# Optimization experiments

Hardware: AMD Instinct MI355X
Metric: run time of the kernel (lower is better)

## Reference

```python
import jax, jax.numpy as jnp
import numpy as np

CLIP_VAL = 32

def setup_inputs() -> dict:
    key = jax.random.key(0)
    ks = jax.random.split(key, 8)
    B, T, D_MODEL, H, DK = 4, 1024, 1024, 16, 64
    s = 0.02  # small init scale, glorot-like magnitude
    return {
        "query": jax.random.normal(ks[0], (B, T, D_MODEL), jnp.float32),
        "value": jax.random.normal(ks[1], (B, T, D_MODEL), jnp.float32),
        "W_Q": jax.random.normal(ks[2], (H, D_MODEL, DK), jnp.float32) * s,
        "W_K": jax.random.normal(ks[3], (H, D_MODEL, DK), jnp.float32) * s,
        "W_V": jax.random.normal(ks[4], (H, D_MODEL, DK), jnp.float32) * s,
        "W_O": jax.random.normal(ks[5], (H, DK, D_MODEL), jnp.float32) * s,
        "emb_Q": jax.random.normal(ks[6], (2 * CLIP_VAL + 1, DK), jnp.float32) * s,
        "emb_S": jax.random.normal(ks[7], (2 * CLIP_VAL + 1, DK), jnp.float32) * s,
    }

def reference(query, value, W_Q, W_K, W_V, W_O, emb_Q, emb_S):
    # query/value: (B, T, D_Model); per-head weights: (H, D_Model, Dk)
    T = query.shape[1]
    Dk = W_Q.shape[-1]
    sqrt_D = jnp.sqrt(jnp.asarray(Dk, query.dtype))

    # relative position index matrix: (T, T) ints in [0, 2*clip]
    tau = jnp.arange(T)
    rel = (jnp.clip(tau[None, :] - tau[:, None], -CLIP_VAL, CLIP_VAL) + CLIP_VAL)
    eQ = emb_Q[rel]  # (T, T, Dk) relative key embedding
    eS = emb_S[rel]  # (T, T, Dv) relative value embedding

    qW = jnp.einsum('btm,hmd->bhtd', query, W_Q)  # (B,H,T,Dk)
    kW = jnp.einsum('btm,hmd->bhtd', value, W_K)
    vW = jnp.einsum('btm,hmd->bhtd', value, W_V)

    # content scores + relative-query bias, both scaled by 1/sqrt(Dk)
    scores = (jnp.einsum('bhtd,bhsd->bhts', qW, kW)
              + jnp.einsum('bhtd,tsd->bhts', qW, eQ)) / sqrt_D
    p = jax.nn.softmax(scores, axis=-1)  # (B,H,T,T)

    # value combination + relative-value term
    heads = (jnp.einsum('bhts,bhsd->bhtd', p, vW)
             + jnp.einsum('bhts,tsd->bhtd', p, eS))

    # per-head output projection then sum over heads
    out = jnp.einsum('bhtd,hdm->btm', heads, W_O)  # (B,T,D_Model)
    return out
```

## Files before the change

### kernel.cpp

```cpp
#include <hip/hip_runtime.h>
#include <math.h>


typedef _Float16 f16;
typedef f16 half8 __attribute__((ext_vector_type(8)));
typedef f16 half4v __attribute__((ext_vector_type(4)));
typedef float f32x4 __attribute__((ext_vector_type(4)));
typedef float f32x16 __attribute__((ext_vector_type(16)));

__global__ __launch_bounds__(256) void prep(
    const float* __restrict__ q, const float* __restrict__ v,
    const float* __restrict__ W0, const float* __restrict__ W1,
    const float* __restrict__ W2, const float* __restrict__ WO,
    f16* __restrict__ q16, f16* __restrict__ Wt16, f16* __restrict__ WOt16) {
    __shared__ float tile[64][65];
    const int bx = blockIdx.x;
    const int t = threadIdx.x;
    if (bx < 8192) {
        int i = (bx * 256 + t) * 4;
        const float* s = (i < 4194304) ? (q + i) : (v + (i - 4194304));
        float4 x = *(const float4*)s;
        half4v h = {(f16)x.x, (f16)x.y, (f16)x.z, (f16)x.w};
        *(half4v*)&q16[i] = h;
        return;
    }
    const int c = t & 63, r4 = t >> 6;
    const int n = t >> 2, kc = (t & 3) * 16;
    if (bx < 8960) {
        const int idx = bx - 8192;
        const int z = idx >> 4, k0 = (idx & 15) * 64;
        const float* src = ((z < 16) ? W0 : (z < 32) ? W1 : W2) + (size_t)(z & 15) * 65536;
        f16* out = Wt16 + (size_t)z * 65536;
#pragma unroll
        for (int p = 0; p < 16; ++p)
            tile[r4 + p * 4][c] = src[(size_t)(k0 + r4 + p * 4) * 64 + c];
        __syncthreads();
        f16 buf[16];
#pragma unroll
        for (int i = 0; i < 16; ++i) buf[i] = (f16)tile[kc + i][n];
        *(half8*)&out[(size_t)n * 1024 + k0 + kc] = *(half8*)&buf[0];
        *(half8*)&out[(size_t)n * 1024 + k0 + kc + 8] = *(half8*)&buf[8];
        return;
    }
    {
        const int idx = bx - 8960;
        const int k0 = (idx & 15) * 64, n0 = (idx >> 4) * 64;
#pragma unroll
        for (int p = 0; p < 16; ++p)
            tile[r4 + p * 4][c] = WO[(size_t)(k0 + r4 + p * 4) * 1024 + n0 + c];
        __syncthreads();
        f16 buf[16];
#pragma unroll
        for (int i = 0; i < 16; ++i) buf[i] = (f16)tile[kc + i][n];
        *(half8*)&WOt16[(size_t)(n0 + n) * 1024 + k0 + kc] = *(half8*)&buf[0];
        *(half8*)&WOt16[(size_t)(n0 + n) * 1024 + k0 + kc + 8] = *(half8*)&buf[8];
    }
}

template <int MODE, int NT, bool DBUF>
__global__ __launch_bounds__(256) void mfma_gemm(
    const f16* __restrict__ Aq, const f16* __restrict__ Av,
    const f16* __restrict__ Bt, float* __restrict__ C,
    f16* __restrict__ oQ, f16* __restrict__ oK, f16* __restrict__ oVt) {
    constexpr int K = 1024;
    constexpr int NI = NT / 32;
    constexpr int LDSZ = (128 + NT) * 64;
    const int n0 = blockIdx.x * NT;
    const int m0 = blockIdx.y * 128;
    const f16* Abase = (MODE == 0) ? ((n0 < 1024) ? Aq : Av) : Aq;

    __shared__ f16 lds[LDSZ * (DBUF ? 2 : 1)];

    const int tid = threadIdx.x;
    const int l = tid & 63, wv = tid >> 6;
    const int rseg = l >> 3;
    const int g = (l & 7) ^ rseg;
    const bool isA = (wv < 2);
    const int rowBase = isA ? (wv & 1) * 64 : (wv & 1) * (NT / 2);
    const int nLoads = isA ? 8 : (NT / 16);
    const f16* gSrc = isA ? (Abase + (size_t)m0 * K) : (Bt + (size_t)n0 * K);
    const f16* gLane = gSrc + (size_t)(rowBase + rseg) * K + g * 8;
    const int ldsRow0 = (isA ? 0 : 128) + rowBase;

    const int fr = l & 15, fq = l >> 4, sw = fr & 7;
    const int mi2 = wv & 1, ni2 = wv >> 1;
    int aOff[NI], bOff[4];
#pragma unroll
    for (int i = 0; i < 4; ++i) bOff[i] = (mi2 * 64 + i * 16 + fr) * 128;
#pragma unroll
    for (int i = 0; i < NI; ++i)
        aOff[i] = (128 + ni2 * (NT / 2) + i * 16 + fr) * 128;

    f32x4 acc[4][NI];
#pragma unroll
    for (int i = 0; i < 4; ++i)
#pragma unroll
        for (int j = 0; j < NI; ++j) acc[i][j] = {0.f, 0.f, 0.f, 0.f};

    auto issue = [&](int k0, int buf) {
        f16* dst = lds + (buf ? LDSZ : 0);
#pragma unroll 8
        for (int i = 0; i < nLoads; ++i) {
            const f16* src = gLane + (size_t)i * 8 * K + k0;
            __builtin_amdgcn_global_load_lds(
                (const __attribute__((address_space(1))) unsigned int*)src,
                (__attribute__((address_space(3))) unsigned int*)
                    &dst[(ldsRow0 + i * 8) * 64], 16, 0, 0);
        }
    };

    if (DBUF) issue(0, 0);
    int it = 0;
    for (int k0 = 0; k0 < K; k0 += 64, ++it) {
        if (!DBUF) issue(k0, 0);
        __syncthreads();
        if (DBUF && k0 + 64 < K) issue(k0 + 64, (it + 1) & 1);
        const char* lp = (const char*)lds + (DBUF ? (it & 1) * (LDSZ * 2) : 0);
#pragma unroll
        for (int kk = 0; kk < 2; ++kk) {
            const int glq = kk * 4 + fq;
            const int sgl = (glq ^ sw) * 16;
            half8 aF[NI], bF[4];
#pragma unroll
            for (int i = 0; i < NI; ++i)
                aF[i] = *(const half8*)(lp + aOff[i] + sgl);
#pragma unroll
            for (int i = 0; i < 4; ++i)
                bF[i] = *(const half8*)(lp + bOff[i] + sgl);
#pragma unroll
            for (int mi = 0; mi < 4; ++mi)
#pragma unroll
                for (int ni = 0; ni < NI; ++ni)
                    acc[mi][ni] = __builtin_amdgcn_mfma_f32_16x16x32_f16(
                        aF[ni], bF[mi], acc[mi][ni], 0, 0, 0);
        }
        if (!DBUF) __syncthreads();
    }
#pragma unroll
    for (int mi = 0; mi < 4; ++mi) {
        const int m = m0 + mi2 * 64 + mi * 16 + fr;
#pragma unroll
        for (int ni = 0; ni < NI; ++ni) {
            const int n = n0 + ni2 * (NT / 2) + ni * 16 + 4 * fq;
            if (MODE == 1) {
                *(f32x4*)(C + (size_t)m * 1024 + n) = acc[mi][ni];
            } else {
                const int w = n >> 10, h = (n >> 6) & 15, d = n & 63;
                const int b = m >> 10, t = m & 1023;
                const size_t bh = (size_t)(b * 16 + h);
                f32x4 a = acc[mi][ni];
                if (w == 0) {
                    half4v hv = {(f16)(a[0] * 0.125f), (f16)(a[1] * 0.125f),
                                 (f16)(a[2] * 0.125f), (f16)(a[3] * 0.125f)};
                    *(half4v*)&oQ[bh * 65536 + (size_t)t * 64 + d] = hv;
                } else if (w == 1) {
                    half4v hv = {(f16)a[0], (f16)a[1], (f16)a[2], (f16)a[3]};
                    *(half4v*)&oK[bh * 65536 + (size_t)t * 64 + d] = hv;
                } else {
#pragma unroll
                    for (int r = 0; r < 4; ++r)
                        oVt[bh * 65536 + (size_t)(d + r) * 1024 + t] = (f16)a[r];
                }
            }
        }
    }
}

__global__ __launch_bounds__(256, 2) void attn_kernel(
    const f16* __restrict__ q16a, const f16* __restrict__ k16,
    const f16* __restrict__ vt16, const float* __restrict__ embQ,
    const float* __restrict__ embS, f16* __restrict__ heads16) {
    const int bh = blockIdx.x;
    const int t0 = blockIdx.y * 128;
    const f16* qg = q16a + (size_t)bh * 65536;
    const f16* kg = k16 + (size_t)bh * 65536;
    const f16* vg = vt16 + (size_t)bh * 65536;

    __shared__ f16 Kt[2][4096];
    __shared__ f16 Vt[2][4096];
    __shared__ f16 qEl[66 * 136];
    __shared__ f16 band[128 * 72];
    __shared__ float e64s[64];

    const int tid = threadIdx.x;
    const int wv = tid >> 6, lane = tid & 63;
    const int tl32 = lane & 31, h = lane >> 5;
    const int tl = wv * 32 + tl32;
    const int tg = t0 + tl;

    auto stageKV = [&](int j0, int buf) {
#pragma unroll
        for (int i = 0; i < 2; ++i) {
            const int rt = wv * 16 + i * 8 + (lane >> 3);
            const int g = (lane & 7) ^ (rt & 7);
            __builtin_amdgcn_global_load_lds(
                (const __attribute__((address_space(1))) unsigned int*)
                    (kg + (size_t)(j0 + rt) * 64 + g * 8),
                (__attribute__((address_space(3))) unsigned int*)
                    &Kt[buf][(wv * 16 + i * 8) * 64], 16, 0, 0);
            __builtin_amdgcn_global_load_lds(
                (const __attribute__((address_space(1))) unsigned int*)
                    (vg + (size_t)rt * 1024 + j0 + g * 8),
                (__attribute__((address_space(3))) unsigned int*)
                    &Vt[buf][(wv * 16 + i * 8) * 64], 16, 0, 0);
        }
    };

    half8 qf[4];
#pragma unroll
    for (int ks = 0; ks < 4; ++ks)
        qf[ks] = *(const half8*)&qg[(size_t)tg * 64 + (2 * ks + h) * 8];
    stageKV(0, 0);

    f16* embQs = band;
    for (int idx = tid; idx < 768; idx += 256) {
        const int row = idx >> 3, p = idx & 7, g = p ^ (row & 7);
        half8 hv;
        if (row < 65) {
            const float* s = embQ + row * 64 + g * 8;
#pragma unroll
            for (int j = 0; j < 8; ++j) hv[j] = (f16)s[j];
        } else {
#pragma unroll
            for (int j = 0; j < 8; ++j) hv[j] = (f16)0.f;
        }
        *(half8*)&embQs[row * 64 + p * 8] = hv;
    }
    __syncthreads();
    {
        f32x16 qacc[3];
#pragma unroll
        for (int mt = 0; mt < 3; ++mt)
#pragma unroll
            for (int r = 0; r < 16; ++r) qacc[mt][r] = 0.f;
#pragma unroll
        for (int ks = 0; ks < 4; ++ks)
#pragma unroll
            for (int mt = 0; mt < 3; ++mt) {
                const int row = tl32 + 32 * mt;
                const int p = (2 * ks + h) ^ (row & 7);
                half8 ef = *(const half8*)&embQs[row * 64 + p * 8];
                qacc[mt] = __builtin_amdgcn_mfma_f32_32x32x16_f16(
                    ef, qf[ks], qacc[mt], 0, 0, 0);
            }
        __syncthreads();
#pragma unroll
        for (int mt = 0; mt < 3; ++mt)
#pragma unroll
            for (int r = 0; r < 16; ++r) {
                const int rr = (r & 3) + 8 * (r >> 2) + 4 * h + 32 * mt;
                if (rr < 65) qEl[rr * 136 + tl] = (f16)qacc[mt][r];
            }
    }
    for (int idx = tid; idx < 1152; idx += 256) {
        half8 hv;
#pragma unroll
        for (int j = 0; j < 8; ++j) hv[j] = (f16)(-1.0e4f);
        *(half8*)&band[idx * 8] = hv;
    }
    if (tid < 64) e64s[tid] = embS[64 * 64 + tid];
    __syncthreads();
    const float qE0 = (float)qEl[tl];
    const float qE64 = (float)qEl[64 * 136 + tl];

    float rs = 0.f, rsL = 0.f;
    f32x16 oacc[2];
#pragma unroll
    for (int dt = 0; dt < 2; ++dt)
#pragma unroll
        for (int r = 0; r < 16; ++r) oacc[dt][r] = 0.f;

    for (int jt = 0; jt < 16; ++jt) {
        const int j0 = jt * 64;
        __syncthreads();
        if (jt < 15) stageKV(j0 + 64, (jt + 1) & 1);
        const f16* Ktc = Kt[jt & 1];
        const f16* Vtc = Vt[jt & 1];
        f32x16 sacc[2];
#pragma unroll
        for (int mt = 0; mt < 2; ++mt)
#pragma unroll
            for (int r = 0; r < 16; ++r) sacc[mt][r] = 0.f;
#pragma unroll
        for (int ks = 0; ks < 4; ++ks)
#pragma unroll
            for (int mt = 0; mt < 2; ++mt) {
                const int row = tl32 + 32 * mt;
                const int p = (2 * ks + h) ^ (row & 7);
                half8 kf = *(const half8*)&Ktc[row * 64 + p * 8];
                sacc[mt] = __builtin_amdgcn_mfma_f32_32x32x16_f16(
                    kf, qf[ks], sacc[mt], 0, 0, 0);
            }
        const int dj = j0 - t0;
        if (dj <= -128 || dj >= 192) {
            const float bias = (dj < 0) ? qE0 : qE64;
            float ts = 0.f;
#pragma unroll
            for (int mt = 0; mt < 2; ++mt)
#pragma unroll
                for (int r = 0; r < 16; ++r) {
                    float pe = __expf(sacc[mt][r] + bias);
                    sacc[mt][r] = pe; ts += pe;
                }
            rs += ts;
            if (dj < 0) rsL += ts;
        } else {
#pragma unroll
            for (int mt = 0; mt < 2; ++mt)
#pragma unroll
                for (int r = 0; r < 16; ++r) {
                    const int sg = j0 + 32 * mt + (r & 3) + 8 * (r >> 2) + 4 * h;
                    const int ds = sg - tg;
                    const int dc = ds < -32 ? -32 : (ds > 32 ? 32 : ds);
                    float v = sacc[mt][r] + (float)qEl[(dc + 32) * 136 + tl];
                    if (ds >= -31 && ds <= 31) band[tl * 72 + ds + 31] = (f16)v;
                    float pe = __expf(v);
                    sacc[mt][r] = pe; rs += pe;
                    if (ds <= -32) rsL += pe;
                }
        }
#pragma unroll
        for (int ks = 0; ks < 4; ++ks) {
            const int mtile = ks >> 1, rb = (ks & 1) * 8;
            float ex[4];
#pragma unroll
            for (int c = 0; c < 4; ++c) {
                float send = (h == 0) ? sacc[mtile][rb + 4 + c]
                                      : sacc[mtile][rb + c];
                ex[c] = __shfl_xor(send, 32);
            }
            half8 pf;
#pragma unroll
            for (int j = 0; j < 4; ++j)
                pf[j] = (f16)((h == 0) ? sacc[mtile][rb + j] : ex[j]);
#pragma unroll
            for (int j = 0; j < 4; ++j)
                pf[4 + j] = (f16)((h == 0) ? ex[j] : sacc[mtile][rb + 4 + j]);
#pragma unroll
            for (int dt = 0; dt < 2; ++dt) {
                const int row = tl32 + 32 * dt;
                const int p = (2 * ks + h) ^ (row & 7);
                half8 vf = *(const half8*)&Vtc[row * 64 + p * 8];
                oacc[dt] = __builtin_amdgcn_mfma_f32_32x32x16_f16(
                    vf, pf, oacc[dt], 0, 0, 0);
            }
        }
    }
    rs += __shfl_xor(rs, 32);
    rsL += __shfl_xor(rsL, 32);
    float sumBand = 0.f;
#pragma unroll
    for (int c = 0; c < 4; ++c) {
        const int kb = 32 * h + 8 * c;
        half8 bv = *(const half8*)&band[tl * 72 + kb];
        half8 ev;
#pragma unroll
        for (int j = 0; j < 8; ++j) {
            const int k = kb + j;
            float v;
            if (k == 63) v = rsL;
            else { v = __expf((float)bv[j]); sumBand += v; }
            ev[j] = (f16)v;
        }
        *(half8*)&band[tl * 72 + kb] = ev;
    }
    sumBand += __shfl_xor(sumBand, 32);
    const float sumR = rs - rsL - sumBand;
    for (int idx = tid; idx < 512; idx += 256) {
        const int d = idx >> 3, p = idx & 7, g = p ^ (d & 7);
        half8 hv;
#pragma unroll
        for (int j = 0; j < 8; ++j) {
            const int k = g * 8 + j;
            hv[j] = (f16)embS[((k == 63) ? 0 : (k + 1)) * 64 + d];
        }
        *(half8*)&Kt[0][d * 64 + p * 8] = hv;
    }
    __syncthreads();
#pragma unroll
    for (int ks = 0; ks < 4; ++ks) {
        half8 pf = *(const half8*)&band[tl * 72 + 16 * ks + 8 * h];
#pragma unroll
        for (int dt = 0; dt < 2; ++dt) {
            const int row = tl32 + 32 * dt;
            const int p = (2 * ks + h) ^ (row & 7);
            half8 ef = *(const half8*)&Kt[0][row * 64 + p * 8];
            oacc[dt] = __builtin_amdgcn_mfma_f32_32x32x16_f16(
                ef, pf, oacc[dt], 0, 0, 0);
        }
    }
    __syncthreads();
    const float inv = 1.0f / rs;
#pragma unroll
    for (int dt = 0; dt < 2; ++dt)
#pragma unroll
        for (int r = 0; r < 16; ++r) {
            const int d = (r & 3) + 8 * (r >> 2) + 4 * h + 32 * dt;
            band[tl * 72 + d] = (f16)((oacc[dt][r] + sumR * e64s[d]) * inv);
        }
    __syncthreads();
    const int b = bh >> 4, hh = bh & 15;
    const int row = tid >> 1, cb = (tid & 1) * 32;
    f16* dst = heads16 + ((size_t)(b * 1024 + t0 + row) * 1024) + hh * 64 + cb;
#pragma unroll
    for (int c = 0; c < 4; ++c)
        *(half8*)&dst[c * 8] = *(const half8*)&band[row * 72 + cb + c * 8];
}

extern "C" void kernel_launch(void* const* d_in, const int* in_sizes, int n_in,
                              void* d_out, int out_size, void* d_ws, size_t ws_size,
                              hipStream_t stream) {
    const float* query = (const float*)d_in[0];
    const float* value = (const float*)d_in[1];
    const float* WQ   = (const float*)d_in[2];
    const float* WK   = (const float*)d_in[3];
    const float* WV   = (const float*)d_in[4];
    const float* WO   = (const float*)d_in[5];
    const float* embQ = (const float*)d_in[6];
    const float* embS = (const float*)d_in[7];
    float* out = (float*)d_out;

    f16* w0    = (f16*)d_ws;
    f16* q16   = w0;
    f16* v16   = w0 + 4194304;
    f16* Wt16  = w0 + 8388608;
    f16* WOt16 = w0 + 11534336;
    f16* q16a  = w0 + 12582912;
    f16* k16   = w0 + 16777216;
    f16* vt16  = w0 + 20971520;
    f16* h16   = w0 + 25165824;

    prep<<<9216, 256, 0, stream>>>(query, value, WQ, WK, WV, WO,
                                   q16, Wt16, WOt16);
    mfma_gemm<0, 128, false><<<dim3(24, 32), 256, 0, stream>>>(
        q16, v16, Wt16, nullptr, q16a, k16, vt16);
    attn_kernel<<<dim3(64, 8), 256, 0, stream>>>(q16a, k16, vt16, embQ, embS, h16);
    mfma_gemm<1, 64, true><<<dim3(16, 32), 256, 0, stream>>>(
        h16, h16, WOt16, out, nullptr, nullptr, nullptr);
}
```

Before: 207.0 us.

## Split attention key range across wave pairs with 64-row query tiles

Each block now handles 64 queries instead of 128. Its four waves form two pairs that cover alternating 64-key tiles, and the partial sums and output accumulators are merged through shared memory at the end. K and V fragments are read straight from global memory instead of being staged in double-buffered LDS, which removes the per-tile barriers, and s_setprio is raised around the MFMA sections. The aim is to double the grid and occupancy (launch bounds go to 4) and drop the synchronisation. The cost is uncoalesced, cache-dependent global loads for K and V plus an extra reduction step.

```diff
diff --git a/kernel.cpp b/kernel.cpp
--- a/kernel.cpp
+++ b/kernel.cpp
@@ -166,53 +166,35 @@
     }
 }
 
-__global__ __launch_bounds__(256, 2) void attn_kernel(
+__global__ __launch_bounds__(256, 4) void attn_kernel(
     const f16* __restrict__ q16a, const f16* __restrict__ k16,
     const f16* __restrict__ vt16, const float* __restrict__ embQ,
     const float* __restrict__ embS, f16* __restrict__ heads16) {
     const int bh = blockIdx.x;
-    const int t0 = blockIdx.y * 128;
+    const int t0 = blockIdx.y * 64;
     const f16* qg = q16a + (size_t)bh * 65536;
     const f16* kg = k16 + (size_t)bh * 65536;
     const f16* vg = vt16 + (size_t)bh * 65536;
 
-    __shared__ f16 Kt[2][4096];
-    __shared__ f16 Vt[2][4096];
-    __shared__ f16 qEl[66 * 136];
-    __shared__ f16 band[128 * 72];
+    __shared__ __align__(16) f16 smem[9360];
+    __shared__ float Obuf[4096];
+    __shared__ float redS[128];
     __shared__ float e64s[64];
+    f16* qEl = smem;
+    f16* band = smem + 4752;
 
     const int tid = threadIdx.x;
     const int wv = tid >> 6, lane = tid & 63;
     const int tl32 = lane & 31, h = lane >> 5;
-    const int tl = wv * 32 + tl32;
+    const int tl = (wv & 1) * 32 + tl32;
+    const int sh = wv >> 1;
     const int tg = t0 + tl;
-
-    auto stageKV = [&](int j0, int buf) {
-#pragma unroll
-        for (int i = 0; i < 2; ++i) {
-            const int rt = wv * 16 + i * 8 + (lane >> 3);
-            const int g = (lane & 7) ^ (rt & 7);
-            __builtin_amdgcn_global_load_lds(
-                (const __attribute__((address_space(1))) unsigned int*)
-                    (kg + (size_t)(j0 + rt) * 64 + g * 8),
-                (__attribute__((address_space(3))) unsigned int*)
-                    &Kt[buf][(wv * 16 + i * 8) * 64], 16, 0, 0);
-            __builtin_amdgcn_global_load_lds(
-                (const __attribute__((address_space(1))) unsigned int*)
-                    (vg + (size_t)rt * 1024 + j0 + g * 8),
-                (__attribute__((address_space(3))) unsigned int*)
-                    &Vt[buf][(wv * 16 + i * 8) * 64], 16, 0, 0);
-        }
-    };
 
     half8 qf[4];
 #pragma unroll
     for (int ks = 0; ks < 4; ++ks)
         qf[ks] = *(const half8*)&qg[(size_t)tg * 64 + (2 * ks + h) * 8];
-    stageKV(0, 0);
-
-    f16* embQs = band;
+
     for (int idx = tid; idx < 768; idx += 256) {
         const int row = idx >> 3, p = idx & 7, g = p ^ (row & 7);
         half8 hv;
@@ -224,35 +206,37 @@
 #pragma unroll
             for (int j = 0; j < 8; ++j) hv[j] = (f16)0.f;
         }
-        *(half8*)&embQs[row * 64 + p * 8] = hv;
-    }
-    __syncthreads();
-    {
-        f32x16 qacc[3];
-#pragma unroll
-        for (int mt = 0; mt < 3; ++mt)
-#pragma unroll
-            for (int r = 0; r < 16; ++r) qacc[mt][r] = 0.f;
+        *(half8*)&smem[row * 64 + p * 8] = hv;
+    }
+    __syncthreads();
+    f32x16 qacc[3];
+#pragma unroll
+    for (int mt = 0; mt < 3; ++mt)
+#pragma unroll
+        for (int r = 0; r < 16; ++r) qacc[mt][r] = 0.f;
+    if (wv < 2) {
 #pragma unroll
         for (int ks = 0; ks < 4; ++ks)
 #pragma unroll
             for (int mt = 0; mt < 3; ++mt) {
                 const int row = tl32 + 32 * mt;
                 const int p = (2 * ks + h) ^ (row & 7);
-                half8 ef = *(const half8*)&embQs[row * 64 + p * 8];
+                half8 ef = *(const half8*)&smem[row * 64 + p * 8];
                 qacc[mt] = __builtin_amdgcn_mfma_f32_32x32x16_f16(
                     ef, qf[ks], qacc[mt], 0, 0, 0);
             }
-        __syncthreads();
+    }
+    __syncthreads();
+    if (wv < 2) {
 #pragma unroll
         for (int mt = 0; mt < 3; ++mt)
 #pragma unroll
             for (int r = 0; r < 16; ++r) {
                 const int rr = (r & 3) + 8 * (r >> 2) + 4 * h + 32 * mt;
-                if (rr < 65) qEl[rr * 136 + tl] = (f16)qacc[mt][r];
-            }
-    }
-    for (int idx = tid; idx < 1152; idx += 256) {
+                if (rr < 65) qEl[rr * 72 + tl] = (f16)qacc[mt][r];
+            }
+    }
+    for (int idx = tid; idx < 576; idx += 256) {
         half8 hv;
 #pragma unroll
         for (int j = 0; j < 8; ++j) hv[j] = (f16)(-1.0e4f);
@@ -261,7 +245,7 @@
     if (tid < 64) e64s[tid] = embS[64 * 64 + tid];
     __syncthreads();
     const float qE0 = (float)qEl[tl];
-    const float qE64 = (float)qEl[64 * 136 + tl];
+    const float qE64 = (float)qEl[64 * 72 + tl];
 
     float rs = 0.f, rsL = 0.f;
     f32x16 oacc[2];
@@ -270,29 +254,29 @@
 #pragma unroll
         for (int r = 0; r < 16; ++r) oacc[dt][r] = 0.f;
 
-    for (int jt = 0; jt < 16; ++jt) {
+#pragma unroll 1
+    for (int jj = 0; jj < 8; ++jj) {
+        const int jt = 2 * jj + sh;
         const int j0 = jt * 64;
-        __syncthreads();
-        if (jt < 15) stageKV(j0 + 64, (jt + 1) & 1);
-        const f16* Ktc = Kt[jt & 1];
-        const f16* Vtc = Vt[jt & 1];
         f32x16 sacc[2];
 #pragma unroll
         for (int mt = 0; mt < 2; ++mt)
 #pragma unroll
             for (int r = 0; r < 16; ++r) sacc[mt][r] = 0.f;
+        __builtin_amdgcn_s_setprio(1);
 #pragma unroll
         for (int ks = 0; ks < 4; ++ks)
 #pragma unroll
             for (int mt = 0; mt < 2; ++mt) {
                 const int row = tl32 + 32 * mt;
-                const int p = (2 * ks + h) ^ (row & 7);
-                half8 kf = *(const half8*)&Ktc[row * 64 + p * 8];
+                half8 kf = *(const half8*)&kg[(size_t)(j0 + row) * 64 +
+                                              (2 * ks + h) * 8];
                 sacc[mt] = __builtin_amdgcn_mfma_f32_32x32x16_f16(
                     kf, qf[ks], sacc[mt], 0, 0, 0);
             }
+        __builtin_amdgcn_s_setprio(0);
         const int dj = j0 - t0;
-        if (dj <= -128 || dj >= 192) {
+        if (dj <= -128 || dj >= 128) {
             const float bias = (dj < 0) ? qE0 : qE64;
             float ts = 0.f;
 #pragma unroll
@@ -312,7 +296,7 @@
                     const int sg = j0 + 32 * mt + (r & 3) + 8 * (r >> 2) + 4 * h;
                     const int ds = sg - tg;
                     const int dc = ds < -32 ? -32 : (ds > 32 ? 32 : ds);
-                    float v = sacc[mt][r] + (float)qEl[(dc + 32) * 136 + tl];
+                    float v = sacc[mt][r] + (float)qEl[(dc + 32) * 72 + tl];
                     if (ds >= -31 && ds <= 31) band[tl * 72 + ds + 31] = (f16)v;
                     float pe = __expf(v);
                     sacc[mt][r] = pe; rs += pe;
@@ -336,75 +320,103 @@
 #pragma unroll
             for (int j = 0; j < 4; ++j)
                 pf[4 + j] = (f16)((h == 0) ? ex[j] : sacc[mtile][rb + 4 + j]);
+            __builtin_amdgcn_s_setprio(1);
+#pragma unroll
+            for (int dt = 0; dt < 2; ++dt) {
+                const int row = tl32 + 32 * dt;
+                half8 vf = *(const half8*)&vg[(size_t)row * 1024 + j0 +
+                                              (2 * ks + h) * 8];
+                oacc[dt] = __builtin_amdgcn_mfma_f32_32x32x16_f16(
+                    vf, pf, oacc[dt], 0, 0, 0);
+            }
+            __builtin_amdgcn_s_setprio(0);
+        }
+    }
+    rs += __shfl_xor(rs, 32);
+    rsL += __shfl_xor(rsL, 32);
+    if (wv >= 2) {
+        if (h == 0) { redS[tl] = rs; redS[64 + tl] = rsL; }
+#pragma unroll
+        for (int dt = 0; dt < 2; ++dt)
+#pragma unroll
+            for (int r = 0; r < 16; ++r) {
+                const int d = (r & 3) + 8 * (r >> 2) + 4 * h + 32 * dt;
+                Obuf[d * 64 + tl] = oacc[dt][r];
+            }
+    }
+    __syncthreads();
+    float sumR = 0.f, inv = 0.f;
+    if (wv < 2) {
+        rs += redS[tl];
+        rsL += redS[64 + tl];
+#pragma unroll
+        for (int dt = 0; dt < 2; ++dt)
+#pragma unroll
+            for (int r = 0; r < 16; ++r) {
+                const int d = (r & 3) + 8 * (r >> 2) + 4 * h + 32 * dt;
+                oacc[dt][r] += Obuf[d * 64 + tl];
+            }
+        float sumBand = 0.f;
+#pragma unroll
+        for (int c = 0; c < 4; ++c) {
+            const int kb = 32 * h + 8 * c;
+            half8 bv = *(const half8*)&band[tl * 72 + kb];
+            half8 ev;
+#pragma unroll
+            for (int j = 0; j < 8; ++j) {
+                const int k = kb + j;
+                float v;
+                if (k == 63) v = rsL;
+                else { v = __expf((float)bv[j]); sumBand += v; }
+                ev[j] = (f16)v;
+            }
+            *(half8*)&band[tl * 72 + kb] = ev;
+        }
+        sumBand += __shfl_xor(sumBand, 32);
+        sumR = rs - rsL - sumBand;
+        inv = 1.0f / rs;
+    }
+    for (int idx = tid; idx < 512; idx += 256) {
+        const int d = idx >> 3, p = idx & 7, g = p ^ (d & 7);
+        half8 hv;
+#pragma unroll
+        for (int j = 0; j < 8; ++j) {
+            const int k = g * 8 + j;
+            hv[j] = (f16)embS[((k == 63) ? 0 : (k + 1)) * 64 + d];
+        }
+        *(half8*)&qEl[d * 64 + p * 8] = hv;
+    }
+    __syncthreads();
+    if (wv < 2) {
+#pragma unroll
+        for (int ks = 0; ks < 4; ++ks) {
+            half8 pf = *(const half8*)&band[tl * 72 + 16 * ks + 8 * h];
 #pragma unroll
             for (int dt = 0; dt < 2; ++dt) {
                 const int row = tl32 + 32 * dt;
                 const int p = (2 * ks + h) ^ (row & 7);
-                half8 vf = *(const half8*)&Vtc[row * 64 + p * 8];
+                half8 ef = *(const half8*)&qEl[row * 64 + p * 8];
                 oacc[dt] = __builtin_amdgcn_mfma_f32_32x32x16_f16(
-                    vf, pf, oacc[dt], 0, 0, 0);
-            }
-        }
-    }
-    rs += __shfl_xor(rs, 32);
-    rsL += __shfl_xor(rsL, 32);
-    float sumBand = 0.f;
-#pragma unroll
-    for (int c = 0; c < 4; ++c) {
-        const int kb = 32 * h + 8 * c;
-        half8 bv = *(const half8*)&band[tl * 72 + kb];
-        half8 ev;
-#pragma unroll
-        for (int j = 0; j < 8; ++j) {
-            const int k = kb + j;
-            float v;
-            if (k == 63) v = rsL;
-            else { v = __expf((float)bv[j]); sumBand += v; }
-            ev[j] = (f16)v;
-        }
-        *(half8*)&band[tl * 72 + kb] = ev;
-    }
-    sumBand += __shfl_xor(sumBand, 32);
-    const float sumR = rs - rsL - sumBand;
-    for (int idx = tid; idx < 512; idx += 256) {
-        const int d = idx >> 3, p = idx & 7, g = p ^ (d & 7);
-        half8 hv;
-#pragma unroll
-        for (int j = 0; j < 8; ++j) {
-            const int k = g * 8 + j;
-            hv[j] = (f16)embS[((k == 63) ? 0 : (k + 1)) * 64 + d];
-        }
-        *(half8*)&Kt[0][d * 64 + p * 8] = hv;
-    }
-    __syncthreads();
-#pragma unroll
-    for (int ks = 0; ks < 4; ++ks) {
-        half8 pf = *(const half8*)&band[tl * 72 + 16 * ks + 8 * h];
-#pragma unroll
-        for (int dt = 0; dt < 2; ++dt) {
-            const int row = tl32 + 32 * dt;
-            const int p = (2 * ks + h) ^ (row & 7);
-            half8 ef = *(const half8*)&Kt[0][row * 64 + p * 8];
-            oacc[dt] = __builtin_amdgcn_mfma_f32_32x32x16_f16(
-                ef, pf, oacc[dt], 0, 0, 0);
-        }
-    }
-    __syncthreads();
-    const float inv = 1.0f / rs;
-#pragma unroll
-    for (int dt = 0; dt < 2; ++dt)
-#pragma unroll
-        for (int r = 0; r < 16; ++r) {
-            const int d = (r & 3) + 8 * (r >> 2) + 4 * h + 32 * dt;
-            band[tl * 72 + d] = (f16)((oacc[dt][r] + sumR * e64s[d]) * inv);
-        }
+                    ef, pf, oacc[dt], 0, 0, 0);
+            }
+        }
+    }
+    __syncthreads();
+    if (wv < 2) {
+#pragma unroll
+        for (int dt = 0; dt < 2; ++dt)
+#pragma unroll
+            for (int r = 0; r < 16; ++r) {
+                const int d = (r & 3) + 8 * (r >> 2) + 4 * h + 32 * dt;
+                band[tl * 72 + d] = (f16)((oacc[dt][r] + sumR * e64s[d]) * inv);
+            }
+    }
     __syncthreads();
     const int b = bh >> 4, hh = bh & 15;
-    const int row = tid >> 1, cb = (tid & 1) * 32;
+    const int row = tid >> 2, cb = (tid & 3) * 16;
     f16* dst = heads16 + ((size_t)(b * 1024 + t0 + row) * 1024) + hh * 64 + cb;
-#pragma unroll
-    for (int c = 0; c < 4; ++c)
-        *(half8*)&dst[c * 8] = *(const half8*)&band[row * 72 + cb + c * 8];
+    *(half8*)&dst[0] = *(const half8*)&band[row * 72 + cb];
+    *(half8*)&dst[8] = *(const half8*)&band[row * 72 + cb + 8];
 }
 
 extern "C" void kernel_launch(void* const* d_in, const int* in_sizes, int n_in,
@@ -434,7 +446,7 @@
                                    q16, Wt16, WOt16);
     mfma_gemm<0, 128, false><<<dim3(24, 32), 256, 0, stream>>>(
         q16, v16, Wt16, nullptr, q16a, k16, vt16);
-    attn_kernel<<<dim3(64, 8), 256, 0, stream>>>(q16a, k16, vt16, embQ, embS, h16);
+    attn_kernel<<<dim3(64, 16), 256, 0, stream>>>(q16a, k16, vt16, embQ, embS, h16);
     mfma_gemm<1, 64, true><<<dim3(16, 32), 256, 0, stream>>>(
         h16, h16, WOt16, out, nullptr, nullptr, nullptr);
 }
```

Result: slower. 246.7 us (+19.2%).

## Split attention key range across two wave groups with 512-thread blocks

Applied to the files above, without the earlier changes.

The attention kernel now runs 512 threads, and two groups of four waves each process alternate 64-key tiles of every 128-key step. Double-buffered staging is replaced by a single shared buffer holding both halves, loaded synchronously between iterations. Partial outputs and row sums from the second group are reduced through shared memory before the band/relative-value epilogue, which runs on the first group only. This aims to raise wave-level parallelism per block and latency hiding, but it removes overlap of loads with compute and adds extra barriers and a reduction step.

```diff
diff --git a/kernel.cpp b/kernel.cpp
--- a/kernel.cpp
+++ b/kernel.cpp
@@ -166,7 +166,7 @@
     }
 }
 
-__global__ __launch_bounds__(256, 2) void attn_kernel(
+__global__ __launch_bounds__(512, 4) void attn_kernel(
     const f16* __restrict__ q16a, const f16* __restrict__ k16,
     const f16* __restrict__ vt16, const float* __restrict__ embQ,
     const float* __restrict__ embS, f16* __restrict__ heads16) {
@@ -176,33 +176,36 @@
     const f16* kg = k16 + (size_t)bh * 65536;
     const f16* vg = vt16 + (size_t)bh * 65536;
 
-    __shared__ f16 Kt[2][4096];
-    __shared__ f16 Vt[2][4096];
-    __shared__ f16 qEl[66 * 136];
-    __shared__ f16 band[128 * 72];
+    __shared__ __align__(16) f16 kvs[16384];
+    __shared__ __align__(16) f16 qEl[66 * 136];
+    __shared__ __align__(16) f16 band[128 * 72];
+    __shared__ float redS[256];
     __shared__ float e64s[64];
 
     const int tid = threadIdx.x;
     const int wv = tid >> 6, lane = tid & 63;
     const int tl32 = lane & 31, h = lane >> 5;
-    const int tl = wv * 32 + tl32;
+    const int tcg = wv & 3, par = wv >> 2;
+    const int tl = tcg * 32 + tl32;
     const int tg = t0 + tl;
 
-    auto stageKV = [&](int j0, int buf) {
-#pragma unroll
-        for (int i = 0; i < 2; ++i) {
-            const int rt = wv * 16 + i * 8 + (lane >> 3);
+    auto stageKV = [&](int i8) {
+        const int j0 = i8 * 128 + par * 64;
+#pragma unroll
+        for (int k = 0; k < 2; ++k) {
+            const int rr = tcg * 16 + k * 8;
+            const int rt = rr + (lane >> 3);
             const int g = (lane & 7) ^ (rt & 7);
             __builtin_amdgcn_global_load_lds(
                 (const __attribute__((address_space(1))) unsigned int*)
                     (kg + (size_t)(j0 + rt) * 64 + g * 8),
                 (__attribute__((address_space(3))) unsigned int*)
-                    &Kt[buf][(wv * 16 + i * 8) * 64], 16, 0, 0);
+                    &kvs[par * 4096 + rr * 64], 16, 0, 0);
             __builtin_amdgcn_global_load_lds(
                 (const __attribute__((address_space(1))) unsigned int*)
                     (vg + (size_t)rt * 1024 + j0 + g * 8),
                 (__attribute__((address_space(3))) unsigned int*)
-                    &Vt[buf][(wv * 16 + i * 8) * 64], 16, 0, 0);
+                    &kvs[8192 + par * 4096 + rr * 64], 16, 0, 0);
         }
     };
 
@@ -210,10 +213,10 @@
 #pragma unroll
     for (int ks = 0; ks < 4; ++ks)
         qf[ks] = *(const half8*)&qg[(size_t)tg * 64 + (2 * ks + h) * 8];
-    stageKV(0, 0);
+    stageKV(0);
 
     f16* embQs = band;
-    for (int idx = tid; idx < 768; idx += 256) {
+    for (int idx = tid; idx < 768; idx += 512) {
         const int row = idx >> 3, p = idx & 7, g = p ^ (row & 7);
         half8 hv;
         if (row < 65) {
@@ -228,31 +231,51 @@
     }
     __syncthreads();
     {
-        f32x16 qacc[3];
-#pragma unroll
-        for (int mt = 0; mt < 3; ++mt)
-#pragma unroll
-            for (int r = 0; r < 16; ++r) qacc[mt][r] = 0.f;
-#pragma unroll
-        for (int ks = 0; ks < 4; ++ks)
-#pragma unroll
-            for (int mt = 0; mt < 3; ++mt) {
-                const int row = tl32 + 32 * mt;
+        if (par == 0) {
+            f32x16 qacc[2];
+#pragma unroll
+            for (int mt = 0; mt < 2; ++mt)
+#pragma unroll
+                for (int r = 0; r < 16; ++r) qacc[mt][r] = 0.f;
+#pragma unroll
+            for (int ks = 0; ks < 4; ++ks)
+#pragma unroll
+                for (int mt = 0; mt < 2; ++mt) {
+                    const int row = tl32 + 32 * mt;
+                    const int p = (2 * ks + h) ^ (row & 7);
+                    half8 ef = *(const half8*)&embQs[row * 64 + p * 8];
+                    qacc[mt] = __builtin_amdgcn_mfma_f32_32x32x16_f16(
+                        ef, qf[ks], qacc[mt], 0, 0, 0);
+                }
+            __syncthreads();
+#pragma unroll
+            for (int mt = 0; mt < 2; ++mt)
+#pragma unroll
+                for (int r = 0; r < 16; ++r) {
+                    const int rr = (r & 3) + 8 * (r >> 2) + 4 * h + 32 * mt;
+                    qEl[rr * 136 + tl] = (f16)qacc[mt][r];
+                }
+        } else {
+            f32x16 qacc;
+#pragma unroll
+            for (int r = 0; r < 16; ++r) qacc[r] = 0.f;
+#pragma unroll
+            for (int ks = 0; ks < 4; ++ks) {
+                const int row = tl32 + 64;
                 const int p = (2 * ks + h) ^ (row & 7);
                 half8 ef = *(const half8*)&embQs[row * 64 + p * 8];
-                qacc[mt] = __builtin_amdgcn_mfma_f32_32x32x16_f16(
-                    ef, qf[ks], qacc[mt], 0, 0, 0);
-            }
-        __syncthreads();
-#pragma unroll
-        for (int mt = 0; mt < 3; ++mt)
+                qacc = __builtin_amdgcn_mfma_f32_32x32x16_f16(
+                    ef, qf[ks], qacc, 0, 0, 0);
+            }
+            __syncthreads();
 #pragma unroll
             for (int r = 0; r < 16; ++r) {
-                const int rr = (r & 3) + 8 * (r >> 2) + 4 * h + 32 * mt;
-                if (rr < 65) qEl[rr * 136 + tl] = (f16)qacc[mt][r];
-            }
-    }
-    for (int idx = tid; idx < 1152; idx += 256) {
+                const int rr = (r & 3) + 8 * (r >> 2) + 4 * h + 64;
+                if (rr < 65) qEl[rr * 136 + tl] = (f16)qacc[r];
+            }
+        }
+    }
+    for (int idx = tid; idx < 1152; idx += 512) {
         half8 hv;
 #pragma unroll
         for (int j = 0; j < 8; ++j) hv[j] = (f16)(-1.0e4f);
@@ -270,12 +293,11 @@
 #pragma unroll
         for (int r = 0; r < 16; ++r) oacc[dt][r] = 0.f;
 
-    for (int jt = 0; jt < 16; ++jt) {
-        const int j0 = jt * 64;
-        __syncthreads();
-        if (jt < 15) stageKV(j0 + 64, (jt + 1) & 1);
-        const f16* Ktc = Kt[jt & 1];
-        const f16* Vtc = Vt[jt & 1];
+#pragma unroll 1
+    for (int it8 = 0; it8 < 8; ++it8) {
+        const int j0 = it8 * 128 + par * 64;
+        const f16* Ktc = kvs + par * 4096;
+        const f16* Vtc = kvs + 8192 + par * 4096;
         f32x16 sacc[2];
 #pragma unroll
         for (int mt = 0; mt < 2; ++mt)
@@ -345,66 +367,100 @@
                     vf, pf, oacc[dt], 0, 0, 0);
             }
         }
+        __syncthreads();
+        if (it8 < 7) {
+            stageKV(it8 + 1);
+            __syncthreads();
+        }
     }
     rs += __shfl_xor(rs, 32);
     rsL += __shfl_xor(rsL, 32);
-    float sumBand = 0.f;
-#pragma unroll
-    for (int c = 0; c < 4; ++c) {
-        const int kb = 32 * h + 8 * c;
-        half8 bv = *(const half8*)&band[tl * 72 + kb];
-        half8 ev;
-#pragma unroll
-        for (int j = 0; j < 8; ++j) {
-            const int k = kb + j;
-            float v;
-            if (k == 63) v = rsL;
-            else { v = __expf((float)bv[j]); sumBand += v; }
-            ev[j] = (f16)v;
-        }
-        *(half8*)&band[tl * 72 + kb] = ev;
-    }
-    sumBand += __shfl_xor(sumBand, 32);
-    const float sumR = rs - rsL - sumBand;
-    for (int idx = tid; idx < 512; idx += 256) {
-        const int d = idx >> 3, p = idx & 7, g = p ^ (d & 7);
+    if (par == 1) {
+        if (h == 0) { redS[tl] = rs; redS[128 + tl] = rsL; }
+        float* Obuf = (float*)kvs;
+#pragma unroll
+        for (int dt = 0; dt < 2; ++dt)
+#pragma unroll
+            for (int r = 0; r < 16; ++r) {
+                const int d = (r & 3) + 8 * (r >> 2) + 4 * h + 32 * dt;
+                Obuf[d * 128 + tl] = oacc[dt][r];
+            }
+    }
+    {
+        const int d = tid >> 3, p = tid & 7, g = p ^ (d & 7);
         half8 hv;
 #pragma unroll
         for (int j = 0; j < 8; ++j) {
             const int k = g * 8 + j;
             hv[j] = (f16)embS[((k == 63) ? 0 : (k + 1)) * 64 + d];
         }
-        *(half8*)&Kt[0][d * 64 + p * 8] = hv;
-    }
-    __syncthreads();
-#pragma unroll
-    for (int ks = 0; ks < 4; ++ks) {
-        half8 pf = *(const half8*)&band[tl * 72 + 16 * ks + 8 * h];
-#pragma unroll
-        for (int dt = 0; dt < 2; ++dt) {
-            const int row = tl32 + 32 * dt;
-            const int p = (2 * ks + h) ^ (row & 7);
-            half8 ef = *(const half8*)&Kt[0][row * 64 + p * 8];
-            oacc[dt] = __builtin_amdgcn_mfma_f32_32x32x16_f16(
-                ef, pf, oacc[dt], 0, 0, 0);
-        }
-    }
-    __syncthreads();
-    const float inv = 1.0f / rs;
-#pragma unroll
-    for (int dt = 0; dt < 2; ++dt)
-#pragma unroll
-        for (int r = 0; r < 16; ++r) {
-            const int d = (r & 3) + 8 * (r >> 2) + 4 * h + 32 * dt;
-            band[tl * 72 + d] = (f16)((oacc[dt][r] + sumR * e64s[d]) * inv);
-        }
+        *(half8*)&qEl[d * 64 + p * 8] = hv;
+    }
+    __syncthreads();
+    float sumR = 0.f, inv = 0.f;
+    if (par == 0) {
+        rs += redS[tl];
+        rsL += redS[128 + tl];
+        const float* Obuf = (const float*)kvs;
+#pragma unroll
+        for (int dt = 0; dt < 2; ++dt)
+#pragma unroll
+            for (int r = 0; r < 16; ++r) {
+                const int d = (r & 3) + 8 * (r >> 2) + 4 * h + 32 * dt;
+                oacc[dt][r] += Obuf[d * 128 + tl];
+            }
+        float sumBand = 0.f;
+#pragma unroll
+        for (int c = 0; c < 4; ++c) {
+            const int kb = 32 * h + 8 * c;
+            half8 bv = *(const half8*)&band[tl * 72 + kb];
+            half8 ev;
+#pragma unroll
+            for (int j = 0; j < 8; ++j) {
+                const int k = kb + j;
+                float v;
+                if (k == 63) v = rsL;
+                else { v = __expf((float)bv[j]); sumBand += v; }
+                ev[j] = (f16)v;
+            }
+            *(half8*)&band[tl * 72 + kb] = ev;
+        }
+        sumBand += __shfl_xor(sumBand, 32);
+        sumR = rs - rsL - sumBand;
+        inv = 1.0f / rs;
+    }
+    __syncthreads();
+    if (par == 0) {
+#pragma unroll
+        for (int ks = 0; ks < 4; ++ks) {
+            half8 pf = *(const half8*)&band[tl * 72 + 16 * ks + 8 * h];
+#pragma unroll
+            for (int dt = 0; dt < 2; ++dt) {
+                const int row = tl32 + 32 * dt;
+                const int p = (2 * ks + h) ^ (row & 7);
+                half8 ef = *(const half8*)&qEl[row * 64 + p * 8];
+                oacc[dt] = __builtin_amdgcn_mfma_f32_32x32x16_f16(
+                    ef, pf, oacc[dt], 0, 0, 0);
+            }
+        }
+    }
+    __syncthreads();
+    if (par == 0) {
+        const float invv = inv;
+#pragma unroll
+        for (int dt = 0; dt < 2; ++dt)
+#pragma unroll
+            for (int r = 0; r < 16; ++r) {
+                const int d = (r & 3) + 8 * (r >> 2) + 4 * h + 32 * dt;
+                band[tl * 72 + d] = (f16)((oacc[dt][r] + sumR * e64s[d]) * invv);
+            }
+    }
     __syncthreads();
     const int b = bh >> 4, hh = bh & 15;
-    const int row = tid >> 1, cb = (tid & 1) * 32;
+    const int row = tid >> 2, cb = (tid & 3) * 16;
     f16* dst = heads16 + ((size_t)(b * 1024 + t0 + row) * 1024) + hh * 64 + cb;
-#pragma unroll
-    for (int c = 0; c < 4; ++c)
-        *(half8*)&dst[c * 8] = *(const half8*)&band[row * 72 + cb + c * 8];
+    *(half8*)&dst[0] = *(const half8*)&band[row * 72 + cb];
+    *(half8*)&dst[8] = *(const half8*)&band[row * 72 + cb + 8];
 }
 
 extern "C" void kernel_launch(void* const* d_in, const int* in_sizes, int n_in,
@@ -434,7 +490,7 @@
                                    q16, Wt16, WOt16);
     mfma_gemm<0, 128, false><<<dim3(24, 32), 256, 0, stream>>>(
         q16, v16, Wt16, nullptr, q16a, k16, vt16);
-    attn_kernel<<<dim3(64, 8), 256, 0, stream>>>(q16a, k16, vt16, embQ, embS, h16);
+    attn_kernel<<<dim3(64, 8), 512, 0, stream>>>(q16a, k16, vt16, embQ, embS, h16);
     mfma_gemm<1, 64, true><<<dim3(16, 32), 256, 0, stream>>>(
         h16, h16, WOt16, out, nullptr, nullptr, nullptr);
 }
```

Result: slower. 216.8 us (+4.8%).

## Move attention band buffer to global scratch to cut LDS and raise occupancy

Applied to the files above, without the earlier changes.

Moves the per-row score band out of shared memory into a global scratch buffer that reuses the q16 workspace. Shared K/V/embedding buffers are merged into one aliased array, and the later band and output staging reuse it. The -1e4 band initialisation is replaced by an explicit bounds check on the band position. This lowers LDS use per block so launch bounds can ask for three blocks per CU, at the cost of global-memory traffic for band writes and reads and tighter register limits.

```diff
diff --git a/kernel.cpp b/kernel.cpp
--- a/kernel.cpp
+++ b/kernel.cpp
@@ -166,20 +166,20 @@
     }
 }
 
-__global__ __launch_bounds__(256, 2) void attn_kernel(
+__global__ __launch_bounds__(256, 3) void attn_kernel(
     const f16* __restrict__ q16a, const f16* __restrict__ k16,
     const f16* __restrict__ vt16, const float* __restrict__ embQ,
-    const float* __restrict__ embS, f16* __restrict__ heads16) {
+    const float* __restrict__ embS, f16* __restrict__ bandG,
+    f16* __restrict__ heads16) {
     const int bh = blockIdx.x;
     const int t0 = blockIdx.y * 128;
     const f16* qg = q16a + (size_t)bh * 65536;
     const f16* kg = k16 + (size_t)bh * 65536;
     const f16* vg = vt16 + (size_t)bh * 65536;
-
-    __shared__ f16 Kt[2][4096];
-    __shared__ f16 Vt[2][4096];
-    __shared__ f16 qEl[66 * 136];
-    __shared__ f16 band[128 * 72];
+    f16* bandB = bandG + (size_t)(bh * 8 + blockIdx.y) * 8192;
+
+    __shared__ __align__(16) f16 kv[16384];
+    __shared__ __align__(16) f16 qEl[66 * 136];
     __shared__ float e64s[64];
 
     const int tid = threadIdx.x;
@@ -197,12 +197,12 @@
                 (const __attribute__((address_space(1))) unsigned int*)
                     (kg + (size_t)(j0 + rt) * 64 + g * 8),
                 (__attribute__((address_space(3))) unsigned int*)
-                    &Kt[buf][(wv * 16 + i * 8) * 64], 16, 0, 0);
+                    &kv[buf * 4096 + (wv * 16 + i * 8) * 64], 16, 0, 0);
             __builtin_amdgcn_global_load_lds(
                 (const __attribute__((address_space(1))) unsigned int*)
                     (vg + (size_t)rt * 1024 + j0 + g * 8),
                 (__attribute__((address_space(3))) unsigned int*)
-                    &Vt[buf][(wv * 16 + i * 8) * 64], 16, 0, 0);
+                    &kv[8192 + buf * 4096 + (wv * 16 + i * 8) * 64], 16, 0, 0);
         }
     };
 
@@ -212,7 +212,6 @@
         qf[ks] = *(const half8*)&qg[(size_t)tg * 64 + (2 * ks + h) * 8];
     stageKV(0, 0);
 
-    f16* embQs = band;
     for (int idx = tid; idx < 768; idx += 256) {
         const int row = idx >> 3, p = idx & 7, g = p ^ (row & 7);
         half8 hv;
@@ -224,7 +223,9 @@
 #pragma unroll
             for (int j = 0; j < 8; ++j) hv[j] = (f16)0.f;
         }
-        *(half8*)&embQs[row * 64 + p * 8] = hv;
+        f16* base = (row < 64) ? (kv + 4096 + row * 64)
+                               : (kv + 12288 + (row - 64) * 64);
+        *(half8*)&base[p * 8] = hv;
     }
     __syncthreads();
     {
@@ -239,7 +240,9 @@
             for (int mt = 0; mt < 3; ++mt) {
                 const int row = tl32 + 32 * mt;
                 const int p = (2 * ks + h) ^ (row & 7);
-                half8 ef = *(const half8*)&embQs[row * 64 + p * 8];
+                const f16* ebase = (mt < 2) ? (kv + 4096 + row * 64)
+                                            : (kv + 12288 + (row - 64) * 64);
+                half8 ef = *(const half8*)&ebase[p * 8];
                 qacc[mt] = __builtin_amdgcn_mfma_f32_32x32x16_f16(
                     ef, qf[ks], qacc[mt], 0, 0, 0);
             }
@@ -251,12 +254,6 @@
                 const int rr = (r & 3) + 8 * (r >> 2) + 4 * h + 32 * mt;
                 if (rr < 65) qEl[rr * 136 + tl] = (f16)qacc[mt][r];
             }
-    }
-    for (int idx = tid; idx < 1152; idx += 256) {
-        half8 hv;
-#pragma unroll
-        for (int j = 0; j < 8; ++j) hv[j] = (f16)(-1.0e4f);
-        *(half8*)&band[idx * 8] = hv;
     }
     if (tid < 64) e64s[tid] = embS[64 * 64 + tid];
     __syncthreads();
@@ -274,8 +271,8 @@
         const int j0 = jt * 64;
         __syncthreads();
         if (jt < 15) stageKV(j0 + 64, (jt + 1) & 1);
-        const f16* Ktc = Kt[jt & 1];
-        const f16* Vtc = Vt[jt & 1];
+        const f16* Ktc = kv + (jt & 1) * 4096;
+        const f16* Vtc = kv + 8192 + (jt & 1) * 4096;
         f32x16 sacc[2];
 #pragma unroll
         for (int mt = 0; mt < 2; ++mt)
@@ -313,7 +310,7 @@
                     const int ds = sg - tg;
                     const int dc = ds < -32 ? -32 : (ds > 32 ? 32 : ds);
                     float v = sacc[mt][r] + (float)qEl[(dc + 32) * 136 + tl];
-                    if (ds >= -31 && ds <= 31) band[tl * 72 + ds + 31] = (f16)v;
+                    if (ds >= -31 && ds <= 31) bandB[tl * 64 + ds + 31] = (f16)v;
                     float pe = __expf(v);
                     sacc[mt][r] = pe; rs += pe;
                     if (ds <= -32) rsL += pe;
@@ -348,21 +345,33 @@
     }
     rs += __shfl_xor(rs, 32);
     rsL += __shfl_xor(rsL, 32);
+    __syncthreads();
+    f16* ovB = kv;
+    f16* eSt = kv + 9216;
     float sumBand = 0.f;
 #pragma unroll
     for (int c = 0; c < 4; ++c) {
         const int kb = 32 * h + 8 * c;
-        half8 bv = *(const half8*)&band[tl * 72 + kb];
+        half8 bv = *(const half8*)&bandB[tl * 64 + kb];
         half8 ev;
 #pragma unroll
         for (int j = 0; j < 8; ++j) {
             const int k = kb + j;
             float v;
-            if (k == 63) v = rsL;
-            else { v = __expf((float)bv[j]); sumBand += v; }
+            if (k == 63) {
+                v = rsL;
+            } else {
+                const int s_of = tg - 31 + k;
+                if ((unsigned)s_of < 1024u) {
+                    v = __expf((float)bv[j]);
+                    sumBand += v;
+                } else {
+                    v = 0.f;
+                }
+            }
             ev[j] = (f16)v;
         }
-        *(half8*)&band[tl * 72 + kb] = ev;
+        *(half8*)&ovB[tl * 72 + kb] = ev;
     }
     sumBand += __shfl_xor(sumBand, 32);
     const float sumR = rs - rsL - sumBand;
@@ -374,17 +383,17 @@
             const int k = g * 8 + j;
             hv[j] = (f16)embS[((k == 63) ? 0 : (k + 1)) * 64 + d];
         }
-        *(half8*)&Kt[0][d * 64 + p * 8] = hv;
+        *(half8*)&eSt[d * 64 + p * 8] = hv;
     }
     __syncthreads();
 #pragma unroll
     for (int ks = 0; ks < 4; ++ks) {
-        half8 pf = *(const half8*)&band[tl * 72 + 16 * ks + 8 * h];
+        half8 pf = *(const half8*)&ovB[tl * 72 + 16 * ks + 8 * h];
 #pragma unroll
         for (int dt = 0; dt < 2; ++dt) {
             const int row = tl32 + 32 * dt;
             const int p = (2 * ks + h) ^ (row & 7);
-            half8 ef = *(const half8*)&Kt[0][row * 64 + p * 8];
+            half8 ef = *(const half8*)&eSt[row * 64 + p * 8];
             oacc[dt] = __builtin_amdgcn_mfma_f32_32x32x16_f16(
                 ef, pf, oacc[dt], 0, 0, 0);
         }
@@ -396,7 +405,7 @@
 #pragma unroll
         for (int r = 0; r < 16; ++r) {
             const int d = (r & 3) + 8 * (r >> 2) + 4 * h + 32 * dt;
-            band[tl * 72 + d] = (f16)((oacc[dt][r] + sumR * e64s[d]) * inv);
+            ovB[tl * 72 + d] = (f16)((oacc[dt][r] + sumR * e64s[d]) * inv);
         }
     __syncthreads();
     const int b = bh >> 4, hh = bh & 15;
@@ -404,7 +413,7 @@
     f16* dst = heads16 + ((size_t)(b * 1024 + t0 + row) * 1024) + hh * 64 + cb;
 #pragma unroll
     for (int c = 0; c < 4; ++c)
-        *(half8*)&dst[c * 8] = *(const half8*)&band[row * 72 + cb + c * 8];
+        *(half8*)&dst[c * 8] = *(const half8*)&ovB[row * 72 + cb + c * 8];
 }
 
 extern "C" void kernel_launch(void* const* d_in, const int* in_sizes, int n_in,
@@ -429,12 +438,14 @@
     f16* k16   = w0 + 16777216;
     f16* vt16  = w0 + 20971520;
     f16* h16   = w0 + 25165824;
+    f16* bandG = q16;
 
     prep<<<9216, 256, 0, stream>>>(query, value, WQ, WK, WV, WO,
                                    q16, Wt16, WOt16);
     mfma_gemm<0, 128, false><<<dim3(24, 32), 256, 0, stream>>>(
         q16, v16, Wt16, nullptr, q16a, k16, vt16);
-    attn_kernel<<<dim3(64, 8), 256, 0, stream>>>(q16a, k16, vt16, embQ, embS, h16);
+    attn_kernel<<<dim3(64, 8), 256, 0, stream>>>(q16a, k16, vt16, embQ, embS,
+                                                 bandG, h16);
     mfma_gemm<1, 64, true><<<dim3(16, 32), 256, 0, stream>>>(
         h16, h16, WOt16, out, nullptr, nullptr, nullptr);
 }
```

Measured after the change: 218.9 us. 1.06x slower.
